# Kernel tuning notes

Hardware: AMD Instinct MI355X
Metric: run time of the kernel (lower is better)

## Reference

```python
import jax, jax.numpy as jnp
import numpy as np

# 5-tap image-gradient filter (cross-correlation taps, as in F.conv2d)
_K5 = (-1.0 / 12.0, 2.0 / 3.0, 0.0, -2.0 / 3.0, 1.0 / 12.0)
ALPHA = BETA = GAMMA = DELTA = 1.0
MASK_COST = 1.0
ENTROPY_WEIGHT = 1.0


def _pen(x):
    return jnp.sqrt(x + 1e-5)


def _filt_w(x):
    # depthwise 1x5 filter along W, padding 2 (matches F.conv2d(x, kernel_gx, padding=(0,2)))
    W = x.shape[-1]
    xp = jnp.pad(x, ((0, 0), (0, 0), (0, 0), (2, 2)))
    out = _K5[0] * xp[..., 0:W]
    for j in range(1, 5):
        out = out + _K5[j] * xp[..., j:j + W]
    return out


def _filt_h(x):
    # depthwise 5x1 filter along H, padding 2
    H = x.shape[-2]
    xp = jnp.pad(x, ((0, 0), (0, 0), (2, 2), (0, 0)))
    out = _K5[0] * xp[..., 0:H, :]
    for j in range(1, 5):
        out = out + _K5[j] * xp[..., j:j + H, :]
    return out


def _warp(img, flow):
    # Bilinear warp: sample img at (x + flow_x, y + flow_y); out-of-range taps contribute 0
    B, C, H, W = img.shape
    xq = jnp.arange(W, dtype=img.dtype)[None, None, :] + flow[:, 0]  # (B,H,W)
    yq = jnp.arange(H, dtype=img.dtype)[None, :, None] + flow[:, 1]
    x0 = jnp.floor(xq)
    y0 = jnp.floor(yq)
    wx1 = xq - x0
    wy1 = yq - y0
    img_flat = img.reshape(B, C, H * W)

    def tap(xi, yi, w):
        valid = (xi >= 0) & (xi <= W - 1) & (yi >= 0) & (yi <= H - 1)
        xc = jnp.clip(xi, 0, W - 1).astype(jnp.int32)
        yc = jnp.clip(yi, 0, H - 1).astype(jnp.int32)
        idx = (yc * W + xc).reshape(B, 1, H * W)
        vals = jnp.take_along_axis(img_flat, jnp.broadcast_to(idx, (B, C, H * W)), axis=2)
        vals = vals.reshape(B, C, H, W)
        return vals * (w * valid.astype(img.dtype))[:, None]

    return (tap(x0, y0, (1 - wx1) * (1 - wy1)) + tap(x0 + 1, y0, wx1 * (1 - wy1))
            + tap(x0, y0 + 1, (1 - wx1) * wy1) + tap(x0 + 1, y0 + 1, wx1 * wy1))


def _border_mask(flow):
    B, _, H, W = flow.shape
    Xp = jnp.arange(W, dtype=flow.dtype)[None, None, :] + flow[:, 0]
    Yp = jnp.arange(H, dtype=flow.dtype)[None, :, None] + flow[:, 1]
    mask_x = jax.nn.sigmoid(Xp + 0.5) * (1.0 - jax.nn.sigmoid(Xp - (W - 0.5)))
    mask_y = jax.nn.sigmoid(Yp + 0.5) * (1.0 - jax.nn.sigmoid(Yp - (H - 0.5)))
    return mask_x * mask_y


def _direction_terms(flow_a, flow_b, img_a, img_b):
    # energy terms for one direction (warping *_b by flow_a)
    mask = _border_mask(flow_a)
    flow_b_warp = _warp(flow_b, flow_a)
    mag = jnp.sum(flow_a ** 2 + flow_b_warp ** 2, axis=1)
    diff = flow_a + flow_b_warp
    occ = 1.0 - jax.nn.sigmoid(jnp.sum(diff ** 2, axis=1) - (0.01 * mag + 0.5))
    mask = mask * occ
    mask_term = MASK_COST * jnp.sum(1.0 - mask, axis=(1, 2)).mean()
    img_b_warp = _warp(img_b, flow_a)
    A = jnp.sum((img_a - img_b_warp) ** 2, axis=1)
    data_term = ALPHA * jnp.sum(_pen(A) * mask, axis=(1, 2)).mean()
    dx = flow_a[..., 1:] - flow_a[..., :-1]
    dy = flow_a[:, :, 1:, :] - flow_a[:, :, :-1, :]
    Bt = (jnp.pad(jnp.sum(dx ** 2, axis=1), ((0, 0), (0, 0), (0, 1)))
          + jnp.pad(jnp.sum(dy ** 2, axis=1), ((0, 0), (0, 1), (0, 0))))
    smooth_term = BETA * jnp.sum(_pen(Bt), axis=(1, 2)).mean()
    Ct = (jnp.sum((_filt_w(img_a) - _filt_w(img_b_warp)) ** 2, axis=1)
          + jnp.sum((_filt_h(img_a) - _filt_h(img_b_warp)) ** 2, axis=1))
    grad_term = GAMMA * jnp.sum(_pen(Ct) * mask, axis=(1, 2)).mean()
    D = jnp.sum(diff ** 2, axis=1)
    fb_part = DELTA * jnp.sum(_pen(D) * mask, axis=(1, 2)).mean()
    return mask_term + data_term + smooth_term + grad_term + fb_part


def _elbo_epe(meanf, log_varf, meanb, log_varb, img1, img2, target, noise_f, noise_b):
    # reparameterized flow samples (Nsamples = 1)
    flowf = meanf + jnp.exp(log_varf / 2.0) * noise_f
    flowb = meanb + jnp.exp(log_varb / 2.0) * noise_b
    energy = (_direction_terms(flowf, flowb, img1, img2)
              + _direction_terms(flowb, flowf, img2, img1))
    entropy = (jnp.sum(log_varf, axis=(1, 2, 3)) / 2
               + jnp.sum(log_varb, axis=(1, 2, 3)) / 2).mean()
    elbo = energy - ENTROPY_WEIGHT * entropy
    epe = jnp.sqrt(jnp.sum((meanf - target) ** 2, axis=1)).mean()
    return elbo, epe


def setup_inputs() -> dict:
    key = jax.random.key(0)
    ks = jax.random.split(key, 9)
    B, H, W = 8, 384, 512
    return {
        "meanf": jax.random.normal(ks[0], (B, 2, H, W), jnp.float32),
        "log_varf": jax.random.normal(ks[1], (B, 2, H, W), jnp.float32),
        "meanb": jax.random.normal(ks[2], (B, 2, H, W), jnp.float32),
        "log_varb": jax.random.normal(ks[3], (B, 2, H, W), jnp.float32),
        "img1": jax.random.uniform(ks[4], (B, 3, H, W), jnp.float32),
        "img2": jax.random.uniform(ks[5], (B, 3, H, W), jnp.float32),
        "target": jax.random.normal(ks[6], (B, 2, H, W), jnp.float32),
        "noise_f": jax.random.normal(ks[7], (B, 2, H, W), jnp.float32),
        "noise_b": jax.random.normal(ks[8], (B, 2, H, W), jnp.float32),
    }


def reference(meanf, log_varf, meanb, log_varb, img1, img2, target, noise_f, noise_b):
    elbo, epe = _elbo_epe(meanf, log_varf, meanb, log_varb, img1, img2, target, noise_f, noise_b)
    return (elbo, epe)
```

## Files before the change

kernel.cpp:

```cpp
#include <hip/hip_runtime.h>
#include <math.h>

#define BATCH 8
#define IH 384
#define IW 512
#define NPIX (IH*IW)
#define BN (BATCH*NPIX)

#define TW 64
#define TH 16
#define RW (TW+4)
#define RH (TH+4)
#define RN (RW*RH)
#define NTX (IW/TW)
#define NTY (IH/TH)
#define NB_DIR (NTX*NTY*BATCH*2)

#define HS 8
#define SH (TH+2*HS)
#define SW (TW+2*HS)
#define SF4 (SW/4)

#define NB_FLOW 1536
#define ENT_OFF NB_DIR
#define EPE_OFF (ENT_OFF + NB_FLOW)
#define PART_FLOATS 8192

__device__ __forceinline__ float frcp_(float x){ return __builtin_amdgcn_rcpf(x); }
__device__ __forceinline__ float fsqrt_(float x){ return __builtin_amdgcn_sqrtf(x); }
__device__ __forceinline__ float sigmoidf_(float x){ return frcp_(1.0f + __expf(-x)); }

__device__ __forceinline__ float block_reduce_sum(float v){
    __shared__ float s[8];
    #pragma unroll
    for (int off=32; off>0; off>>=1) v += __shfl_down(v, off);
    int lane = threadIdx.x & 63, wid = threadIdx.x >> 6;
    if (lane==0) s[wid] = v;
    __syncthreads();
    float t = 0.f;
    if (wid==0){
        int nw = (blockDim.x+63)>>6;
        t = (lane < nw) ? s[lane] : 0.f;
        #pragma unroll
        for (int off=4; off>0; off>>=1) t += __shfl_down(t, off);
    }
    __syncthreads();
    return t;
}

__global__ __launch_bounds__(256)
void flows_kernel(const float* __restrict__ meanf, const float* __restrict__ log_varf,
                  const float* __restrict__ meanb, const float* __restrict__ log_varb,
                  const float* __restrict__ target,
                  const float* __restrict__ noise_f, const float* __restrict__ noise_b,
                  float* __restrict__ flowf, float* __restrict__ flowb,
                  float* __restrict__ part)
{
    int t = blockIdx.x*blockDim.x + threadIdx.x;
    const int NP4 = NPIX/4;
    int b = t / NP4, p4 = t - b*NP4;
    size_t i0 = ((size_t)b*2*NPIX)/4 + p4;
    size_t i1 = i0 + NPIX/4;

    const float4* mf = (const float4*)meanf;  const float4* lf = (const float4*)log_varf;
    const float4* mb = (const float4*)meanb;  const float4* lb = (const float4*)log_varb;
    const float4* nf = (const float4*)noise_f; const float4* nb = (const float4*)noise_b;
    const float4* tg = (const float4*)target;
    float4* ff = (float4*)flowf; float4* fbp = (float4*)flowb;

    float4 lf0 = lf[i0], lf1 = lf[i1], lb0 = lb[i0], lb1 = lb[i1];
    float4 mf0 = mf[i0], mf1 = mf[i1], mb0 = mb[i0], mb1 = mb[i1];
    float4 nf0 = nf[i0], nf1 = nf[i1], nb0 = nb[i0], nb1 = nb[i1];

    float4 o;
    o.x = mf0.x + __expf(0.5f*lf0.x)*nf0.x; o.y = mf0.y + __expf(0.5f*lf0.y)*nf0.y;
    o.z = mf0.z + __expf(0.5f*lf0.z)*nf0.z; o.w = mf0.w + __expf(0.5f*lf0.w)*nf0.w;
    ff[i0] = o;
    o.x = mf1.x + __expf(0.5f*lf1.x)*nf1.x; o.y = mf1.y + __expf(0.5f*lf1.y)*nf1.y;
    o.z = mf1.z + __expf(0.5f*lf1.z)*nf1.z; o.w = mf1.w + __expf(0.5f*lf1.w)*nf1.w;
    ff[i1] = o;
    o.x = mb0.x + __expf(0.5f*lb0.x)*nb0.x; o.y = mb0.y + __expf(0.5f*lb0.y)*nb0.y;
    o.z = mb0.z + __expf(0.5f*lb0.z)*nb0.z; o.w = mb0.w + __expf(0.5f*lb0.w)*nb0.w;
    fbp[i0] = o;
    o.x = mb1.x + __expf(0.5f*lb1.x)*nb1.x; o.y = mb1.y + __expf(0.5f*lb1.y)*nb1.y;
    o.z = mb1.z + __expf(0.5f*lb1.z)*nb1.z; o.w = mb1.w + __expf(0.5f*lb1.w)*nb1.w;
    fbp[i1] = o;

    float ent = (lf0.x+lf0.y+lf0.z+lf0.w) + (lf1.x+lf1.y+lf1.z+lf1.w)
              + (lb0.x+lb0.y+lb0.z+lb0.w) + (lb1.x+lb1.y+lb1.z+lb1.w);

    float4 t0 = tg[i0], t1 = tg[i1];
    float d0, d1, epe = 0.f;
    d0 = mf0.x - t0.x; d1 = mf1.x - t1.x; epe += fsqrt_(d0*d0 + d1*d1);
    d0 = mf0.y - t0.y; d1 = mf1.y - t1.y; epe += fsqrt_(d0*d0 + d1*d1);
    d0 = mf0.z - t0.z; d1 = mf1.z - t1.z; epe += fsqrt_(d0*d0 + d1*d1);
    d0 = mf0.w - t0.w; d1 = mf1.w - t1.w; epe += fsqrt_(d0*d0 + d1*d1);

    float s = block_reduce_sum(ent);
    if (threadIdx.x == 0) part[ENT_OFF + blockIdx.x] = s;
    float s2 = block_reduce_sum(epe);
    if (threadIdx.x == 0) part[EPE_OFF + blockIdx.x] = s2;
}

__global__ __launch_bounds__(256)
void dir_kernel(const float* __restrict__ flowf, const float* __restrict__ flowb,
                const float* __restrict__ img1, const float* __restrict__ img2,
                float* __restrict__ part)
{
    __shared__ float sib[3][SH][SW];
    __shared__ float wlds[3][RH][RW];
    __shared__ float mlds[TH][TW];

    const int dir = blockIdx.z & 1, b = blockIdx.z >> 1;
    const float *pfa, *pfb, *pia, *pib;
    if (dir == 0){ pfa = flowf; pfb = flowb; pia = img1; pib = img2; }
    else         { pfa = flowb; pfb = flowf; pia = img2; pib = img1; }
    pfa += (size_t)b*2*NPIX; pfb += (size_t)b*2*NPIX;
    pia += (size_t)b*3*NPIX; pib += (size_t)b*3*NPIX;

    const int tw0 = blockIdx.x*TW, th0 = blockIdx.y*TH;
    const int tid = threadIdx.x;
    float local = 0.f;

    for (int i = tid; i < 3*SH*SF4; i += 256){
        int c = i / (SH*SF4);
        int rem = i - c*(SH*SF4);
        int r = rem / SF4, c4 = rem - r*SF4;
        int gy = th0 - HS + r;
        int gx = tw0 - HS + 4*c4;
        float4 v = make_float4(0.f, 0.f, 0.f, 0.f);
        if (gy >= 0 && gy < IH && gx >= 0 && gx < IW){
            v = *(const float4*)(pib + (size_t)c*NPIX + gy*IW + gx);
        }
        *(float4*)&sib[c][r][4*c4] = v;
    }
    __syncthreads();

    for (int i = tid; i < RN; i += 256){
        int hh = i / RW, ww = i - hh*RW;
        int gh = th0 + hh - 2, gw = tw0 + ww - 2;
        bool inimg = (gh >= 0) && (gh < IH) && (gw >= 0) && (gw < IW);
        float w0 = 0.f, w1 = 0.f, w2 = 0.f;
        if (inimg){
            int p = gh*IW + gw;
            float fax = pfa[p], fay = pfa[NPIX + p];
            float Xp = (float)gw + fax;
            float Yp = (float)gh + fay;

            float x0f = floorf(Xp), y0f = floorf(Yp);
            float wx1 = Xp - x0f, wy1 = Yp - y0f;
            float wx0 = 1.f - wx1, wy0 = 1.f - wy1;

            float x1f = x0f + 1.f, y1f = y0f + 1.f;
            bool vx0 = (x0f >= 0.f) && (x0f <= (float)(IW-1));
            bool vx1 = (x1f >= 0.f) && (x1f <= (float)(IW-1));
            bool vy0 = (y0f >= 0.f) && (y0f <= (float)(IH-1));
            bool vy1 = (y1f >= 0.f) && (y1f <= (float)(IH-1));
            float xc0 = fminf(fmaxf(x0f, 0.f), (float)(IW-1));
            float xc1 = fminf(fmaxf(x1f, 0.f), (float)(IW-1));
            float yc0 = fminf(fmaxf(y0f, 0.f), (float)(IH-1));
            float yc1 = fminf(fmaxf(y1f, 0.f), (float)(IH-1));
            int ix0 = (int)xc0, ix1 = (int)xc1, iy0 = (int)yc0, iy1 = (int)yc1;
            int idx0 = iy0*IW + ix0, idx1 = iy0*IW + ix1;
            int idx2 = iy1*IW + ix0, idx3 = iy1*IW + ix1;
            float wt0 = (vx0 && vy0) ? wx0*wy0 : 0.f;
            float wt1 = (vx1 && vy0) ? wx1*wy0 : 0.f;
            float wt2 = (vx0 && vy1) ? wx0*wy1 : 0.f;
            float wt3 = (vx1 && vy1) ? wx1*wy1 : 0.f;

            int lx0 = ix0 - (tw0 - HS), ly0 = iy0 - (th0 - HS);
            int lx1 = ix1 - (tw0 - HS), ly1 = iy1 - (th0 - HS);
            bool inwin = (lx0 >= 0) && (lx1 < SW) && (ly0 >= 0) && (ly1 < SH);
            if (inwin){
                int o00 = ly0*SW + lx0, o01 = ly0*SW + lx1;
                int o10 = ly1*SW + lx0, o11 = ly1*SW + lx1;
                const float* s0 = &sib[0][0][0];
                const float* s1 = s0 + SH*SW;
                const float* s2 = s1 + SH*SW;
                w0 = wt0*s0[o00] + wt1*s0[o01] + wt2*s0[o10] + wt3*s0[o11];
                w1 = wt0*s1[o00] + wt1*s1[o01] + wt2*s1[o10] + wt3*s1[o11];
                w2 = wt0*s2[o00] + wt1*s2[o01] + wt2*s2[o10] + wt3*s2[o11];
            } else {
                const float* g1 = pib + NPIX;
                const float* g2 = pib + 2*NPIX;
                w0 = wt0*pib[idx0] + wt1*pib[idx1] + wt2*pib[idx2] + wt3*pib[idx3];
                w1 = wt0*g1[idx0]  + wt1*g1[idx1]  + wt2*g1[idx2]  + wt3*g1[idx3];
                w2 = wt0*g2[idx0]  + wt1*g2[idx1]  + wt2*g2[idx2]  + wt3*g2[idx3];
            }

            bool interior = (hh >= 2) && (hh < RH-2) && (ww >= 2) && (ww < RW-2);
            if (interior){
                float mx = sigmoidf_(Xp + 0.5f) * (1.f - sigmoidf_(Xp - ((float)IW - 0.5f)));
                float my = sigmoidf_(Yp + 0.5f) * (1.f - sigmoidf_(Yp - ((float)IH - 0.5f)));
                float bm = mx * my;

                float fbwx = wt0*pfb[idx0] + wt1*pfb[idx1] + wt2*pfb[idx2] + wt3*pfb[idx3];
                const float* pfb1 = pfb + NPIX;
                float fbwy = wt0*pfb1[idx0] + wt1*pfb1[idx1] + wt2*pfb1[idx2] + wt3*pfb1[idx3];

                float mag = fax*fax + fay*fay + fbwx*fbwx + fbwy*fbwy;
                float dfx = fax + fbwx, dfy = fay + fbwy;
                float D = dfx*dfx + dfy*dfy;
                float occ = 1.f - sigmoidf_(D - (0.01f*mag + 0.5f));
                float mask = bm * occ;
                mlds[hh-2][ww-2] = mask;

                local += (1.f - mask);

                float d0 = pia[p]        - w0;
                float d1 = pia[NPIX+p]   - w1;
                float d2 = pia[2*NPIX+p] - w2;
                local += fsqrt_(d0*d0 + d1*d1 + d2*d2 + 1e-5f) * mask;

                local += fsqrt_(D + 1e-5f) * mask;

                float Bt = 0.f;
                if (gw < IW-1){
                    float e0 = pfa[p+1] - fax;
                    float e1 = pfa[NPIX + p+1] - fay;
                    Bt += e0*e0 + e1*e1;
                }
                if (gh < IH-1){
                    float e0 = pfa[p+IW] - fax;
                    float e1 = pfa[NPIX + p+IW] - fay;
                    Bt += e0*e0 + e1*e1;
                }
                local += fsqrt_(Bt + 1e-5f);
            }
        }
        wlds[0][hh][ww] = w0;
        wlds[1][hh][ww] = w1;
        wlds[2][hh][ww] = w2;
    }
    __syncthreads();

    const float K0 = -1.f/12.f, K1 = 2.f/3.f, K3 = -2.f/3.f, K4 = 1.f/12.f;
    for (int i = tid; i < TW*TH; i += 256){
        int hh = i >> 6, ww = i & 63;
        int gh = th0 + hh, gw = tw0 + ww;
        int lh = hh + 2, lw = ww + 2;
        int p = gh*IW + gw;
        float Ct = 0.f;
        #pragma unroll
        for (int c = 0; c < 3; ++c){
            const float* A_ = pia + (size_t)c*NPIX;
            float gxa = 0.f;
            if (gw >= 2)    gxa += K0*A_[p-2];
            if (gw >= 1)    gxa += K1*A_[p-1];
            if (gw <= IW-2) gxa += K3*A_[p+1];
            if (gw <= IW-3) gxa += K4*A_[p+2];
            float gxw = K0*wlds[c][lh][lw-2] + K1*wlds[c][lh][lw-1]
                      + K3*wlds[c][lh][lw+1] + K4*wlds[c][lh][lw+2];
            float d = gxa - gxw; Ct += d*d;
            float gya = 0.f;
            if (gh >= 2)    gya += K0*A_[p-2*IW];
            if (gh >= 1)    gya += K1*A_[p-IW];
            if (gh <= IH-2) gya += K3*A_[p+IW];
            if (gh <= IH-3) gya += K4*A_[p+2*IW];
            float gyw = K0*wlds[c][lh-2][lw] + K1*wlds[c][lh-1][lw]
                      + K3*wlds[c][lh+1][lw] + K4*wlds[c][lh+2][lw];
            d = gya - gyw; Ct += d*d;
        }
        local += fsqrt_(Ct + 1e-5f) * mlds[hh][ww];
    }

    float s = block_reduce_sum(local);
    if (tid == 0) part[blockIdx.x + NTX*(blockIdx.y + NTY*blockIdx.z)] = s;
}

__global__ __launch_bounds__(256)
void finalize_kernel(const float* __restrict__ part, float* __restrict__ out)
{
    float e = 0.f, ent = 0.f, epe = 0.f;
    for (int i = threadIdx.x; i < NB_DIR; i += 256) e += part[i];
    for (int i = threadIdx.x; i < NB_FLOW; i += 256){
        ent += part[ENT_OFF + i];
        epe += part[EPE_OFF + i];
    }
    e   = block_reduce_sum(e);
    ent = block_reduce_sum(ent);
    epe = block_reduce_sum(epe);
    if (threadIdx.x == 0){
        out[0] = e / (float)BATCH - ent / (2.f * (float)BATCH);
        out[1] = epe / ((float)BATCH * (float)NPIX);
    }
}

extern "C" void kernel_launch(void* const* d_in, const int* in_sizes, int n_in,
                              void* d_out, int out_size, void* d_ws, size_t ws_size,
                              hipStream_t stream)
{
    const float* meanf    = (const float*)d_in[0];
    const float* log_varf = (const float*)d_in[1];
    const float* meanb    = (const float*)d_in[2];
    const float* log_varb = (const float*)d_in[3];
    const float* img1     = (const float*)d_in[4];
    const float* img2     = (const float*)d_in[5];
    const float* target   = (const float*)d_in[6];
    const float* noise_f  = (const float*)d_in[7];
    const float* noise_b  = (const float*)d_in[8];

    float* ws    = (float*)d_ws;
    float* part  = ws;
    float* flowf = ws + PART_FLOATS;
    float* flowb = flowf + 2*(size_t)BN;

    const int threads = 256;

    flows_kernel<<<NB_FLOW, threads, 0, stream>>>(meanf, log_varf, meanb, log_varb,
                                                  target, noise_f, noise_b,
                                                  flowf, flowb, part);

    dim3 grid(NTX, NTY, BATCH*2);
    dir_kernel<<<grid, threads, 0, stream>>>(flowf, flowb, img1, img2, part);

    finalize_kernel<<<1, threads, 0, stream>>>(part, (float*)d_out);
}
```

Baseline: 274.1 us.

## Alias warp scratch onto image window LDS and prefetch flow into registers

After: 267.2 us. 2.5% less time.

```diff
diff --git a/kernel.cpp b/kernel.cpp
--- a/kernel.cpp
+++ b/kernel.cpp
@@ -16,10 +16,13 @@
 #define NTY (IH/TH)
 #define NB_DIR (NTX*NTY*BATCH*2)
 
-#define HS 8
-#define SH (TH+2*HS)
-#define SW (TW+2*HS)
+#define HSX 8
+#define HSY 6
+#define SH (TH+2*HSY)
+#define SW (TW+2*HSX)
 #define SF4 (SW/4)
+#define SMEM_FLOATS (3*SH*SW)
+#define NITER 6
 
 #define NB_FLOW 1536
 #define ENT_OFF NB_DIR
@@ -102,13 +105,12 @@
     if (threadIdx.x == 0) part[EPE_OFF + blockIdx.x] = s2;
 }
 
-__global__ __launch_bounds__(256)
+__global__ __launch_bounds__(256, 5)
 void dir_kernel(const float* __restrict__ flowf, const float* __restrict__ flowb,
                 const float* __restrict__ img1, const float* __restrict__ img2,
                 float* __restrict__ part)
 {
-    __shared__ float sib[3][SH][SW];
-    __shared__ float wlds[3][RH][RW];
+    __shared__ float smem[SMEM_FLOATS];
     __shared__ float mlds[TH][TW];
 
     const int dir = blockIdx.z & 1, b = blockIdx.z >> 1;
@@ -126,115 +128,149 @@
         int c = i / (SH*SF4);
         int rem = i - c*(SH*SF4);
         int r = rem / SF4, c4 = rem - r*SF4;
-        int gy = th0 - HS + r;
-        int gx = tw0 - HS + 4*c4;
+        int gy = th0 - HSY + r;
+        int gx = tw0 - HSX + 4*c4;
         float4 v = make_float4(0.f, 0.f, 0.f, 0.f);
         if (gy >= 0 && gy < IH && gx >= 0 && gx < IW){
             v = *(const float4*)(pib + (size_t)c*NPIX + gy*IW + gx);
         }
-        *(float4*)&sib[c][r][4*c4] = v;
-    }
-    __syncthreads();
-
-    for (int i = tid; i < RN; i += 256){
+        *(float4*)&smem[c*(SH*SW) + r*SW + 4*c4] = v;
+    }
+
+    float rfax[NITER], rfay[NITER];
+    #pragma unroll
+    for (int it = 0; it < NITER; ++it){
+        rfax[it] = 0.f; rfay[it] = 0.f;
+        int i = tid + it*256;
+        if (i < RN){
+            int hh = i / RW, ww = i - hh*RW;
+            int gh = th0 + hh - 2, gw = tw0 + ww - 2;
+            if (gh >= 0 && gh < IH && gw >= 0 && gw < IW){
+                int p = gh*IW + gw;
+                rfax[it] = pfa[p];
+                rfay[it] = pfa[NPIX + p];
+            }
+        }
+    }
+    __syncthreads();
+
+    float rw0[NITER], rw1[NITER], rw2[NITER];
+    #pragma unroll
+    for (int it = 0; it < NITER; ++it){
+        rw0[it] = 0.f; rw1[it] = 0.f; rw2[it] = 0.f;
+        int i = tid + it*256;
+        if (i >= RN) continue;
         int hh = i / RW, ww = i - hh*RW;
         int gh = th0 + hh - 2, gw = tw0 + ww - 2;
         bool inimg = (gh >= 0) && (gh < IH) && (gw >= 0) && (gw < IW);
-        float w0 = 0.f, w1 = 0.f, w2 = 0.f;
-        if (inimg){
-            int p = gh*IW + gw;
-            float fax = pfa[p], fay = pfa[NPIX + p];
-            float Xp = (float)gw + fax;
-            float Yp = (float)gh + fay;
-
-            float x0f = floorf(Xp), y0f = floorf(Yp);
-            float wx1 = Xp - x0f, wy1 = Yp - y0f;
-            float wx0 = 1.f - wx1, wy0 = 1.f - wy1;
-
-            float x1f = x0f + 1.f, y1f = y0f + 1.f;
-            bool vx0 = (x0f >= 0.f) && (x0f <= (float)(IW-1));
-            bool vx1 = (x1f >= 0.f) && (x1f <= (float)(IW-1));
-            bool vy0 = (y0f >= 0.f) && (y0f <= (float)(IH-1));
-            bool vy1 = (y1f >= 0.f) && (y1f <= (float)(IH-1));
-            float xc0 = fminf(fmaxf(x0f, 0.f), (float)(IW-1));
-            float xc1 = fminf(fmaxf(x1f, 0.f), (float)(IW-1));
-            float yc0 = fminf(fmaxf(y0f, 0.f), (float)(IH-1));
-            float yc1 = fminf(fmaxf(y1f, 0.f), (float)(IH-1));
-            int ix0 = (int)xc0, ix1 = (int)xc1, iy0 = (int)yc0, iy1 = (int)yc1;
-            int idx0 = iy0*IW + ix0, idx1 = iy0*IW + ix1;
-            int idx2 = iy1*IW + ix0, idx3 = iy1*IW + ix1;
-            float wt0 = (vx0 && vy0) ? wx0*wy0 : 0.f;
-            float wt1 = (vx1 && vy0) ? wx1*wy0 : 0.f;
-            float wt2 = (vx0 && vy1) ? wx0*wy1 : 0.f;
-            float wt3 = (vx1 && vy1) ? wx1*wy1 : 0.f;
-
-            int lx0 = ix0 - (tw0 - HS), ly0 = iy0 - (th0 - HS);
-            int lx1 = ix1 - (tw0 - HS), ly1 = iy1 - (th0 - HS);
-            bool inwin = (lx0 >= 0) && (lx1 < SW) && (ly0 >= 0) && (ly1 < SH);
-            if (inwin){
-                int o00 = ly0*SW + lx0, o01 = ly0*SW + lx1;
-                int o10 = ly1*SW + lx0, o11 = ly1*SW + lx1;
-                const float* s0 = &sib[0][0][0];
-                const float* s1 = s0 + SH*SW;
-                const float* s2 = s1 + SH*SW;
-                w0 = wt0*s0[o00] + wt1*s0[o01] + wt2*s0[o10] + wt3*s0[o11];
-                w1 = wt0*s1[o00] + wt1*s1[o01] + wt2*s1[o10] + wt3*s1[o11];
-                w2 = wt0*s2[o00] + wt1*s2[o01] + wt2*s2[o10] + wt3*s2[o11];
-            } else {
-                const float* g1 = pib + NPIX;
-                const float* g2 = pib + 2*NPIX;
-                w0 = wt0*pib[idx0] + wt1*pib[idx1] + wt2*pib[idx2] + wt3*pib[idx3];
-                w1 = wt0*g1[idx0]  + wt1*g1[idx1]  + wt2*g1[idx2]  + wt3*g1[idx3];
-                w2 = wt0*g2[idx0]  + wt1*g2[idx1]  + wt2*g2[idx2]  + wt3*g2[idx3];
+        if (!inimg) continue;
+
+        int p = gh*IW + gw;
+        float fax = rfax[it], fay = rfay[it];
+        float Xp = (float)gw + fax;
+        float Yp = (float)gh + fay;
+
+        float x0f = floorf(Xp), y0f = floorf(Yp);
+        float wx1 = Xp - x0f, wy1 = Yp - y0f;
+        float wx0 = 1.f - wx1, wy0 = 1.f - wy1;
+
+        float x1f = x0f + 1.f, y1f = y0f + 1.f;
+        bool vx0 = (x0f >= 0.f) && (x0f <= (float)(IW-1));
+        bool vx1 = (x1f >= 0.f) && (x1f <= (float)(IW-1));
+        bool vy0 = (y0f >= 0.f) && (y0f <= (float)(IH-1));
+        bool vy1 = (y1f >= 0.f) && (y1f <= (float)(IH-1));
+        float xc0 = fminf(fmaxf(x0f, 0.f), (float)(IW-1));
+        float xc1 = fminf(fmaxf(x1f, 0.f), (float)(IW-1));
+        float yc0 = fminf(fmaxf(y0f, 0.f), (float)(IH-1));
+        float yc1 = fminf(fmaxf(y1f, 0.f), (float)(IH-1));
+        int ix0 = (int)xc0, ix1 = (int)xc1, iy0 = (int)yc0, iy1 = (int)yc1;
+        int idx0 = iy0*IW + ix0, idx1 = iy0*IW + ix1;
+        int idx2 = iy1*IW + ix0, idx3 = iy1*IW + ix1;
+        float wt0 = (vx0 && vy0) ? wx0*wy0 : 0.f;
+        float wt1 = (vx1 && vy0) ? wx1*wy0 : 0.f;
+        float wt2 = (vx0 && vy1) ? wx0*wy1 : 0.f;
+        float wt3 = (vx1 && vy1) ? wx1*wy1 : 0.f;
+
+        float w0, w1, w2;
+        int lx0 = ix0 - (tw0 - HSX), ly0 = iy0 - (th0 - HSY);
+        int lx1 = ix1 - (tw0 - HSX), ly1 = iy1 - (th0 - HSY);
+        bool inwin = (lx0 >= 0) && (lx1 < SW) && (ly0 >= 0) && (ly1 < SH);
+        if (inwin){
+            int o00 = ly0*SW + lx0, o01 = ly0*SW + lx1;
+            int o10 = ly1*SW + lx0, o11 = ly1*SW + lx1;
+            const float* s0 = &smem[0];
+            const float* s1 = s0 + SH*SW;
+            const float* s2 = s1 + SH*SW;
+            w0 = wt0*s0[o00] + wt1*s0[o01] + wt2*s0[o10] + wt3*s0[o11];
+            w1 = wt0*s1[o00] + wt1*s1[o01] + wt2*s1[o10] + wt3*s1[o11];
+            w2 = wt0*s2[o00] + wt1*s2[o01] + wt2*s2[o10] + wt3*s2[o11];
+        } else {
+            const float* g1 = pib + NPIX;
+            const float* g2 = pib + 2*NPIX;
+            w0 = wt0*pib[idx0] + wt1*pib[idx1] + wt2*pib[idx2] + wt3*pib[idx3];
+            w1 = wt0*g1[idx0]  + wt1*g1[idx1]  + wt2*g1[idx2]  + wt3*g1[idx3];
+            w2 = wt0*g2[idx0]  + wt1*g2[idx1]  + wt2*g2[idx2]  + wt3*g2[idx3];
+        }
+        rw0[it] = w0; rw1[it] = w1; rw2[it] = w2;
+
+        bool interior = (hh >= 2) && (hh < RH-2) && (ww >= 2) && (ww < RW-2);
+        if (interior){
+            float mx = sigmoidf_(Xp + 0.5f) * (1.f - sigmoidf_(Xp - ((float)IW - 0.5f)));
+            float my = sigmoidf_(Yp + 0.5f) * (1.f - sigmoidf_(Yp - ((float)IH - 0.5f)));
+            float bm = mx * my;
+
+            float fbwx = wt0*pfb[idx0] + wt1*pfb[idx1] + wt2*pfb[idx2] + wt3*pfb[idx3];
+            const float* pfb1 = pfb + NPIX;
+            float fbwy = wt0*pfb1[idx0] + wt1*pfb1[idx1] + wt2*pfb1[idx2] + wt3*pfb1[idx3];
+
+            float mag = fax*fax + fay*fay + fbwx*fbwx + fbwy*fbwy;
+            float dfx = fax + fbwx, dfy = fay + fbwy;
+            float D = dfx*dfx + dfy*dfy;
+            float occ = 1.f - sigmoidf_(D - (0.01f*mag + 0.5f));
+            float mask = bm * occ;
+            mlds[hh-2][ww-2] = mask;
+
+            local += (1.f - mask);
+
+            float d0 = pia[p]        - w0;
+            float d1 = pia[NPIX+p]   - w1;
+            float d2 = pia[2*NPIX+p] - w2;
+            local += fsqrt_(d0*d0 + d1*d1 + d2*d2 + 1e-5f) * mask;
+
+            local += fsqrt_(D + 1e-5f) * mask;
+
+            float Bt = 0.f;
+            if (gw < IW-1){
+                float e0 = pfa[p+1] - fax;
+                float e1 = pfa[NPIX + p+1] - fay;
+                Bt += e0*e0 + e1*e1;
             }
-
-            bool interior = (hh >= 2) && (hh < RH-2) && (ww >= 2) && (ww < RW-2);
-            if (interior){
-                float mx = sigmoidf_(Xp + 0.5f) * (1.f - sigmoidf_(Xp - ((float)IW - 0.5f)));
-                float my = sigmoidf_(Yp + 0.5f) * (1.f - sigmoidf_(Yp - ((float)IH - 0.5f)));
-                float bm = mx * my;
-
-                float fbwx = wt0*pfb[idx0] + wt1*pfb[idx1] + wt2*pfb[idx2] + wt3*pfb[idx3];
-                const float* pfb1 = pfb + NPIX;
-                float fbwy = wt0*pfb1[idx0] + wt1*pfb1[idx1] + wt2*pfb1[idx2] + wt3*pfb1[idx3];
-
-                float mag = fax*fax + fay*fay + fbwx*fbwx + fbwy*fbwy;
-                float dfx = fax + fbwx, dfy = fay + fbwy;
-                float D = dfx*dfx + dfy*dfy;
-                float occ = 1.f - sigmoidf_(D - (0.01f*mag + 0.5f));
-                float mask = bm * occ;
-                mlds[hh-2][ww-2] = mask;
-
-                local += (1.f - mask);
-
-                float d0 = pia[p]        - w0;
-                float d1 = pia[NPIX+p]   - w1;
-                float d2 = pia[2*NPIX+p] - w2;
-                local += fsqrt_(d0*d0 + d1*d1 + d2*d2 + 1e-5f) * mask;
-
-                local += fsqrt_(D + 1e-5f) * mask;
-
-                float Bt = 0.f;
-                if (gw < IW-1){
-                    float e0 = pfa[p+1] - fax;
-                    float e1 = pfa[NPIX + p+1] - fay;
-                    Bt += e0*e0 + e1*e1;
-                }
-                if (gh < IH-1){
-                    float e0 = pfa[p+IW] - fax;
-                    float e1 = pfa[NPIX + p+IW] - fay;
-                    Bt += e0*e0 + e1*e1;
-                }
-                local += fsqrt_(Bt + 1e-5f);
+            if (gh < IH-1){
+                float e0 = pfa[p+IW] - fax;
+                float e1 = pfa[NPIX + p+IW] - fay;
+                Bt += e0*e0 + e1*e1;
             }
-        }
-        wlds[0][hh][ww] = w0;
-        wlds[1][hh][ww] = w1;
-        wlds[2][hh][ww] = w2;
+            local += fsqrt_(Bt + 1e-5f);
+        }
+    }
+    __syncthreads();
+
+    #pragma unroll
+    for (int it = 0; it < NITER; ++it){
+        int i = tid + it*256;
+        if (i < RN){
+            int hh = i / RW, ww = i - hh*RW;
+            smem[0*(RH*RW) + hh*RW + ww] = rw0[it];
+            smem[1*(RH*RW) + hh*RW + ww] = rw1[it];
+            smem[2*(RH*RW) + hh*RW + ww] = rw2[it];
+        }
     }
     __syncthreads();
 
     const float K0 = -1.f/12.f, K1 = 2.f/3.f, K3 = -2.f/3.f, K4 = 1.f/12.f;
+    const float* wl0 = &smem[0];
+    const float* wl1 = wl0 + RH*RW;
+    const float* wl2 = wl1 + RH*RW;
     for (int i = tid; i < TW*TH; i += 256){
         int hh = i >> 6, ww = i & 63;
         int gh = th0 + hh, gw = tw0 + ww;
@@ -244,21 +280,22 @@
         #pragma unroll
         for (int c = 0; c < 3; ++c){
             const float* A_ = pia + (size_t)c*NPIX;
+            const float* Wl = (c == 0) ? wl0 : (c == 1) ? wl1 : wl2;
             float gxa = 0.f;
             if (gw >= 2)    gxa += K0*A_[p-2];
             if (gw >= 1)    gxa += K1*A_[p-1];
             if (gw <= IW-2) gxa += K3*A_[p+1];
             if (gw <= IW-3) gxa += K4*A_[p+2];
-            float gxw = K0*wlds[c][lh][lw-2] + K1*wlds[c][lh][lw-1]
-                      + K3*wlds[c][lh][lw+1] + K4*wlds[c][lh][lw+2];
+            float gxw = K0*Wl[lh*RW + lw-2] + K1*Wl[lh*RW + lw-1]
+                      + K3*Wl[lh*RW + lw+1] + K4*Wl[lh*RW + lw+2];
             float d = gxa - gxw; Ct += d*d;
             float gya = 0.f;
             if (gh >= 2)    gya += K0*A_[p-2*IW];
             if (gh >= 1)    gya += K1*A_[p-IW];
             if (gh <= IH-2) gya += K3*A_[p+IW];
             if (gh <= IH-3) gya += K4*A_[p+2*IW];
-            float gyw = K0*wlds[c][lh-2][lw] + K1*wlds[c][lh-1][lw]
-                      + K3*wlds[c][lh+1][lw] + K4*wlds[c][lh+2][lw];
+            float gyw = K0*Wl[(lh-2)*RW + lw] + K1*Wl[(lh-1)*RW + lw]
+                      + K3*Wl[(lh+1)*RW + lw] + K4*Wl[(lh+2)*RW + lw];
             d = gya - gyw; Ct += d*d;
         }
         local += fsqrt_(Ct + 1e-5f) * mlds[hh][ww];
```

## Split direction kernel into warp and gradient passes with interleaved flow layout

Applied to the files above, without the earlier changes.

After: 247.7 us. 1.11x faster.

```diff
diff --git a/kernel.cpp b/kernel.cpp
--- a/kernel.cpp
+++ b/kernel.cpp
@@ -11,20 +11,25 @@
 #define TH 16
 #define RW (TW+4)
 #define RH (TH+4)
-#define RN (RW*RH)
 #define NTX (IW/TW)
 #define NTY (IH/TH)
-#define NB_DIR (NTX*NTY*BATCH*2)
-
-#define HS 8
-#define SH (TH+2*HS)
-#define SW (TW+2*HS)
+#define NZ  (BATCH*2)
+#define NB_DIR (NTX*NTY*NZ)
+
+#define HSX 8
+#define HSY 6
+#define SH (TH+2*HSY)
+#define SW (TW+2*HSX)
 #define SF4 (SW/4)
 
+#define NITER_A 4
+
 #define NB_FLOW 1536
-#define ENT_OFF NB_DIR
+#define PA_OFF 0
+#define PB_OFF NB_DIR
+#define ENT_OFF (2*NB_DIR)
 #define EPE_OFF (ENT_OFF + NB_FLOW)
-#define PART_FLOATS 8192
+#define PART_FLOATS 16384
 
 __device__ __forceinline__ float frcp_(float x){ return __builtin_amdgcn_rcpf(x); }
 __device__ __forceinline__ float fsqrt_(float x){ return __builtin_amdgcn_sqrtf(x); }
@@ -57,6 +62,7 @@
                   float* __restrict__ part)
 {
     int t = blockIdx.x*blockDim.x + threadIdx.x;
+    if (t < NB_DIR) part[PB_OFF + t] = 0.f;
     const int NP4 = NPIX/4;
     int b = t / NP4, p4 = t - b*NP4;
     size_t i0 = ((size_t)b*2*NPIX)/4 + p4;
@@ -72,19 +78,23 @@
     float4 mf0 = mf[i0], mf1 = mf[i1], mb0 = mb[i0], mb1 = mb[i1];
     float4 nf0 = nf[i0], nf1 = nf[i1], nb0 = nb[i0], nb1 = nb[i1];
 
-    float4 o;
-    o.x = mf0.x + __expf(0.5f*lf0.x)*nf0.x; o.y = mf0.y + __expf(0.5f*lf0.y)*nf0.y;
-    o.z = mf0.z + __expf(0.5f*lf0.z)*nf0.z; o.w = mf0.w + __expf(0.5f*lf0.w)*nf0.w;
-    ff[i0] = o;
-    o.x = mf1.x + __expf(0.5f*lf1.x)*nf1.x; o.y = mf1.y + __expf(0.5f*lf1.y)*nf1.y;
-    o.z = mf1.z + __expf(0.5f*lf1.z)*nf1.z; o.w = mf1.w + __expf(0.5f*lf1.w)*nf1.w;
-    ff[i1] = o;
-    o.x = mb0.x + __expf(0.5f*lb0.x)*nb0.x; o.y = mb0.y + __expf(0.5f*lb0.y)*nb0.y;
-    o.z = mb0.z + __expf(0.5f*lb0.z)*nb0.z; o.w = mb0.w + __expf(0.5f*lb0.w)*nb0.w;
-    fbp[i0] = o;
-    o.x = mb1.x + __expf(0.5f*lb1.x)*nb1.x; o.y = mb1.y + __expf(0.5f*lb1.y)*nb1.y;
-    o.z = mb1.z + __expf(0.5f*lb1.z)*nb1.z; o.w = mb1.w + __expf(0.5f*lb1.w)*nb1.w;
-    fbp[i1] = o;
+    float4 of0, of1;
+    of0.x = mf0.x + __expf(0.5f*lf0.x)*nf0.x; of0.y = mf0.y + __expf(0.5f*lf0.y)*nf0.y;
+    of0.z = mf0.z + __expf(0.5f*lf0.z)*nf0.z; of0.w = mf0.w + __expf(0.5f*lf0.w)*nf0.w;
+    of1.x = mf1.x + __expf(0.5f*lf1.x)*nf1.x; of1.y = mf1.y + __expf(0.5f*lf1.y)*nf1.y;
+    of1.z = mf1.z + __expf(0.5f*lf1.z)*nf1.z; of1.w = mf1.w + __expf(0.5f*lf1.w)*nf1.w;
+    float4 ob0, ob1;
+    ob0.x = mb0.x + __expf(0.5f*lb0.x)*nb0.x; ob0.y = mb0.y + __expf(0.5f*lb0.y)*nb0.y;
+    ob0.z = mb0.z + __expf(0.5f*lb0.z)*nb0.z; ob0.w = mb0.w + __expf(0.5f*lb0.w)*nb0.w;
+    ob1.x = mb1.x + __expf(0.5f*lb1.x)*nb1.x; ob1.y = mb1.y + __expf(0.5f*lb1.y)*nb1.y;
+    ob1.z = mb1.z + __expf(0.5f*lb1.z)*nb1.z; ob1.w = mb1.w + __expf(0.5f*lb1.w)*nb1.w;
+
+    size_t o4 = (size_t)b*(NPIX/2) + (size_t)p4*2;
+    float4 v;
+    v.x = of0.x; v.y = of1.x; v.z = of0.y; v.w = of1.y; ff[o4]   = v;
+    v.x = of0.z; v.y = of1.z; v.z = of0.w; v.w = of1.w; ff[o4+1] = v;
+    v.x = ob0.x; v.y = ob1.x; v.z = ob0.y; v.w = ob1.y; fbp[o4]   = v;
+    v.x = ob0.z; v.y = ob1.z; v.z = ob0.w; v.w = ob1.w; fbp[o4+1] = v;
 
     float ent = (lf0.x+lf0.y+lf0.z+lf0.w) + (lf1.x+lf1.y+lf1.z+lf1.w)
               + (lb0.x+lb0.y+lb0.z+lb0.w) + (lb1.x+lb1.y+lb1.z+lb1.w);
@@ -102,21 +112,30 @@
     if (threadIdx.x == 0) part[EPE_OFF + blockIdx.x] = s2;
 }
 
-__global__ __launch_bounds__(256)
-void dir_kernel(const float* __restrict__ flowf, const float* __restrict__ flowb,
-                const float* __restrict__ img1, const float* __restrict__ img2,
-                float* __restrict__ part)
+__global__ __launch_bounds__(256, 6)
+void dirA_kernel(const float* __restrict__ flowf, const float* __restrict__ flowb,
+                 const float* __restrict__ img1, const float* __restrict__ img2,
+                 float* __restrict__ wimg, float* __restrict__ maskbuf,
+                 float* __restrict__ part)
 {
     __shared__ float sib[3][SH][SW];
-    __shared__ float wlds[3][RH][RW];
-    __shared__ float mlds[TH][TW];
-
-    const int dir = blockIdx.z & 1, b = blockIdx.z >> 1;
-    const float *pfa, *pfb, *pia, *pib;
-    if (dir == 0){ pfa = flowf; pfb = flowb; pia = img1; pib = img2; }
-    else         { pfa = flowb; pfb = flowf; pia = img2; pib = img1; }
-    pfa += (size_t)b*2*NPIX; pfb += (size_t)b*2*NPIX;
-    pia += (size_t)b*3*NPIX; pib += (size_t)b*3*NPIX;
+
+    const int z = blockIdx.z;
+    const int dir = z & 1, b = z >> 1;
+    const float2 *pfa2, *pfb2;
+    const float *pia, *pib;
+    if (dir == 0){
+        pfa2 = (const float2*)flowf + (size_t)b*NPIX;
+        pfb2 = (const float2*)flowb + (size_t)b*NPIX;
+        pia = img1 + (size_t)b*3*NPIX; pib = img2 + (size_t)b*3*NPIX;
+    } else {
+        pfa2 = (const float2*)flowb + (size_t)b*NPIX;
+        pfb2 = (const float2*)flowf + (size_t)b*NPIX;
+        pia = img2 + (size_t)b*3*NPIX; pib = img1 + (size_t)b*3*NPIX;
+    }
+
+    float* wout = wimg + (size_t)z*3*NPIX;
+    float* mout = maskbuf + (size_t)z*NPIX;
 
     const int tw0 = blockIdx.x*TW, th0 = blockIdx.y*TH;
     const int tid = threadIdx.x;
@@ -126,153 +145,198 @@
         int c = i / (SH*SF4);
         int rem = i - c*(SH*SF4);
         int r = rem / SF4, c4 = rem - r*SF4;
-        int gy = th0 - HS + r;
-        int gx = tw0 - HS + 4*c4;
+        int gy = th0 - HSY + r;
+        int gx = tw0 - HSX + 4*c4;
         float4 v = make_float4(0.f, 0.f, 0.f, 0.f);
         if (gy >= 0 && gy < IH && gx >= 0 && gx < IW){
             v = *(const float4*)(pib + (size_t)c*NPIX + gy*IW + gx);
         }
         *(float4*)&sib[c][r][4*c4] = v;
     }
+
+    float2 rfa[NITER_A];
+    #pragma unroll
+    for (int it = 0; it < NITER_A; ++it){
+        int i = tid + it*256;
+        int hh = i >> 6, ww = i & 63;
+        int p = (th0 + hh)*IW + (tw0 + ww);
+        rfa[it] = pfa2[p];
+    }
     __syncthreads();
 
-    for (int i = tid; i < RN; i += 256){
-        int hh = i / RW, ww = i - hh*RW;
-        int gh = th0 + hh - 2, gw = tw0 + ww - 2;
-        bool inimg = (gh >= 0) && (gh < IH) && (gw >= 0) && (gw < IW);
-        float w0 = 0.f, w1 = 0.f, w2 = 0.f;
-        if (inimg){
-            int p = gh*IW + gw;
-            float fax = pfa[p], fay = pfa[NPIX + p];
-            float Xp = (float)gw + fax;
-            float Yp = (float)gh + fay;
-
-            float x0f = floorf(Xp), y0f = floorf(Yp);
-            float wx1 = Xp - x0f, wy1 = Yp - y0f;
-            float wx0 = 1.f - wx1, wy0 = 1.f - wy1;
-
-            float x1f = x0f + 1.f, y1f = y0f + 1.f;
-            bool vx0 = (x0f >= 0.f) && (x0f <= (float)(IW-1));
-            bool vx1 = (x1f >= 0.f) && (x1f <= (float)(IW-1));
-            bool vy0 = (y0f >= 0.f) && (y0f <= (float)(IH-1));
-            bool vy1 = (y1f >= 0.f) && (y1f <= (float)(IH-1));
-            float xc0 = fminf(fmaxf(x0f, 0.f), (float)(IW-1));
-            float xc1 = fminf(fmaxf(x1f, 0.f), (float)(IW-1));
-            float yc0 = fminf(fmaxf(y0f, 0.f), (float)(IH-1));
-            float yc1 = fminf(fmaxf(y1f, 0.f), (float)(IH-1));
-            int ix0 = (int)xc0, ix1 = (int)xc1, iy0 = (int)yc0, iy1 = (int)yc1;
-            int idx0 = iy0*IW + ix0, idx1 = iy0*IW + ix1;
-            int idx2 = iy1*IW + ix0, idx3 = iy1*IW + ix1;
-            float wt0 = (vx0 && vy0) ? wx0*wy0 : 0.f;
-            float wt1 = (vx1 && vy0) ? wx1*wy0 : 0.f;
-            float wt2 = (vx0 && vy1) ? wx0*wy1 : 0.f;
-            float wt3 = (vx1 && vy1) ? wx1*wy1 : 0.f;
-
-            int lx0 = ix0 - (tw0 - HS), ly0 = iy0 - (th0 - HS);
-            int lx1 = ix1 - (tw0 - HS), ly1 = iy1 - (th0 - HS);
-            bool inwin = (lx0 >= 0) && (lx1 < SW) && (ly0 >= 0) && (ly1 < SH);
-            if (inwin){
-                int o00 = ly0*SW + lx0, o01 = ly0*SW + lx1;
-                int o10 = ly1*SW + lx0, o11 = ly1*SW + lx1;
-                const float* s0 = &sib[0][0][0];
-                const float* s1 = s0 + SH*SW;
-                const float* s2 = s1 + SH*SW;
-                w0 = wt0*s0[o00] + wt1*s0[o01] + wt2*s0[o10] + wt3*s0[o11];
-                w1 = wt0*s1[o00] + wt1*s1[o01] + wt2*s1[o10] + wt3*s1[o11];
-                w2 = wt0*s2[o00] + wt1*s2[o01] + wt2*s2[o10] + wt3*s2[o11];
-            } else {
-                const float* g1 = pib + NPIX;
-                const float* g2 = pib + 2*NPIX;
-                w0 = wt0*pib[idx0] + wt1*pib[idx1] + wt2*pib[idx2] + wt3*pib[idx3];
-                w1 = wt0*g1[idx0]  + wt1*g1[idx1]  + wt2*g1[idx2]  + wt3*g1[idx3];
-                w2 = wt0*g2[idx0]  + wt1*g2[idx1]  + wt2*g2[idx2]  + wt3*g2[idx3];
-            }
-
-            bool interior = (hh >= 2) && (hh < RH-2) && (ww >= 2) && (ww < RW-2);
-            if (interior){
-                float mx = sigmoidf_(Xp + 0.5f) * (1.f - sigmoidf_(Xp - ((float)IW - 0.5f)));
-                float my = sigmoidf_(Yp + 0.5f) * (1.f - sigmoidf_(Yp - ((float)IH - 0.5f)));
-                float bm = mx * my;
-
-                float fbwx = wt0*pfb[idx0] + wt1*pfb[idx1] + wt2*pfb[idx2] + wt3*pfb[idx3];
-                const float* pfb1 = pfb + NPIX;
-                float fbwy = wt0*pfb1[idx0] + wt1*pfb1[idx1] + wt2*pfb1[idx2] + wt3*pfb1[idx3];
-
-                float mag = fax*fax + fay*fay + fbwx*fbwx + fbwy*fbwy;
-                float dfx = fax + fbwx, dfy = fay + fbwy;
-                float D = dfx*dfx + dfy*dfy;
-                float occ = 1.f - sigmoidf_(D - (0.01f*mag + 0.5f));
-                float mask = bm * occ;
-                mlds[hh-2][ww-2] = mask;
-
-                local += (1.f - mask);
-
-                float d0 = pia[p]        - w0;
-                float d1 = pia[NPIX+p]   - w1;
-                float d2 = pia[2*NPIX+p] - w2;
-                local += fsqrt_(d0*d0 + d1*d1 + d2*d2 + 1e-5f) * mask;
-
-                local += fsqrt_(D + 1e-5f) * mask;
-
-                float Bt = 0.f;
-                if (gw < IW-1){
-                    float e0 = pfa[p+1] - fax;
-                    float e1 = pfa[NPIX + p+1] - fay;
-                    Bt += e0*e0 + e1*e1;
-                }
-                if (gh < IH-1){
-                    float e0 = pfa[p+IW] - fax;
-                    float e1 = pfa[NPIX + p+IW] - fay;
-                    Bt += e0*e0 + e1*e1;
-                }
-                local += fsqrt_(Bt + 1e-5f);
-            }
-        }
-        wlds[0][hh][ww] = w0;
-        wlds[1][hh][ww] = w1;
-        wlds[2][hh][ww] = w2;
-    }
-    __syncthreads();
-
-    const float K0 = -1.f/12.f, K1 = 2.f/3.f, K3 = -2.f/3.f, K4 = 1.f/12.f;
-    for (int i = tid; i < TW*TH; i += 256){
+    #pragma unroll
+    for (int it = 0; it < NITER_A; ++it){
+        int i = tid + it*256;
         int hh = i >> 6, ww = i & 63;
         int gh = th0 + hh, gw = tw0 + ww;
+        int p = gh*IW + gw;
+        float fax = rfa[it].x, fay = rfa[it].y;
+        float Xp = (float)gw + fax;
+        float Yp = (float)gh + fay;
+
+        float2 f_r = (gw < IW-1) ? pfa2[p+1]  : make_float2(0.f, 0.f);
+        float2 f_d = (gh < IH-1) ? pfa2[p+IW] : make_float2(0.f, 0.f);
+
+        float x0f = floorf(Xp), y0f = floorf(Yp);
+        float wx1 = Xp - x0f, wy1 = Yp - y0f;
+        float wx0 = 1.f - wx1, wy0 = 1.f - wy1;
+
+        float x1f = x0f + 1.f, y1f = y0f + 1.f;
+        bool vx0 = (x0f >= 0.f) && (x0f <= (float)(IW-1));
+        bool vx1 = (x1f >= 0.f) && (x1f <= (float)(IW-1));
+        bool vy0 = (y0f >= 0.f) && (y0f <= (float)(IH-1));
+        bool vy1 = (y1f >= 0.f) && (y1f <= (float)(IH-1));
+        float xc0 = fminf(fmaxf(x0f, 0.f), (float)(IW-1));
+        float xc1 = fminf(fmaxf(x1f, 0.f), (float)(IW-1));
+        float yc0 = fminf(fmaxf(y0f, 0.f), (float)(IH-1));
+        float yc1 = fminf(fmaxf(y1f, 0.f), (float)(IH-1));
+        int ix0 = (int)xc0, ix1 = (int)xc1, iy0 = (int)yc0, iy1 = (int)yc1;
+        int idx0 = iy0*IW + ix0, idx1 = iy0*IW + ix1;
+        int idx2 = iy1*IW + ix0, idx3 = iy1*IW + ix1;
+        float wt0 = (vx0 && vy0) ? wx0*wy0 : 0.f;
+        float wt1 = (vx1 && vy0) ? wx1*wy0 : 0.f;
+        float wt2 = (vx0 && vy1) ? wx0*wy1 : 0.f;
+        float wt3 = (vx1 && vy1) ? wx1*wy1 : 0.f;
+
+        float2 fb0 = pfb2[idx0], fb1 = pfb2[idx1];
+        float2 fb2 = pfb2[idx2], fb3 = pfb2[idx3];
+
+        float a0 = pia[p], a1 = pia[NPIX+p], a2 = pia[2*NPIX+p];
+
+        float w0, w1, w2;
+        int lx0 = ix0 - (tw0 - HSX), ly0 = iy0 - (th0 - HSY);
+        int lx1 = ix1 - (tw0 - HSX), ly1 = iy1 - (th0 - HSY);
+        bool inwin = (lx0 >= 0) && (lx1 < SW) && (ly0 >= 0) && (ly1 < SH);
+        if (inwin){
+            int o00 = ly0*SW + lx0, o01 = ly0*SW + lx1;
+            int o10 = ly1*SW + lx0, o11 = ly1*SW + lx1;
+            const float* s0 = &sib[0][0][0];
+            const float* s1 = s0 + SH*SW;
+            const float* s2 = s1 + SH*SW;
+            w0 = wt0*s0[o00] + wt1*s0[o01] + wt2*s0[o10] + wt3*s0[o11];
+            w1 = wt0*s1[o00] + wt1*s1[o01] + wt2*s1[o10] + wt3*s1[o11];
+            w2 = wt0*s2[o00] + wt1*s2[o01] + wt2*s2[o10] + wt3*s2[o11];
+        } else {
+            const float* g1 = pib + NPIX;
+            const float* g2 = pib + 2*NPIX;
+            w0 = wt0*pib[idx0] + wt1*pib[idx1] + wt2*pib[idx2] + wt3*pib[idx3];
+            w1 = wt0*g1[idx0]  + wt1*g1[idx1]  + wt2*g1[idx2]  + wt3*g1[idx3];
+            w2 = wt0*g2[idx0]  + wt1*g2[idx1]  + wt2*g2[idx2]  + wt3*g2[idx3];
+        }
+
+        float mx = sigmoidf_(Xp + 0.5f) * (1.f - sigmoidf_(Xp - ((float)IW - 0.5f)));
+        float my = sigmoidf_(Yp + 0.5f) * (1.f - sigmoidf_(Yp - ((float)IH - 0.5f)));
+        float bm = mx * my;
+
+        float fbwx = wt0*fb0.x + wt1*fb1.x + wt2*fb2.x + wt3*fb3.x;
+        float fbwy = wt0*fb0.y + wt1*fb1.y + wt2*fb2.y + wt3*fb3.y;
+
+        float mag = fax*fax + fay*fay + fbwx*fbwx + fbwy*fbwy;
+        float dfx = fax + fbwx, dfy = fay + fbwy;
+        float D = dfx*dfx + dfy*dfy;
+        float occ = 1.f - sigmoidf_(D - (0.01f*mag + 0.5f));
+        float mask = bm * occ;
+
+        local += (1.f - mask);
+
+        float d0 = a0 - w0;
+        float d1 = a1 - w1;
+        float d2 = a2 - w2;
+        local += fsqrt_(d0*d0 + d1*d1 + d2*d2 + 1e-5f) * mask;
+
+        local += fsqrt_(D + 1e-5f) * mask;
+
+        float Bt = 0.f;
+        if (gw < IW-1){
+            float e0 = f_r.x - fax;
+            float e1 = f_r.y - fay;
+            Bt += e0*e0 + e1*e1;
+        }
+        if (gh < IH-1){
+            float e0 = f_d.x - fax;
+            float e1 = f_d.y - fay;
+            Bt += e0*e0 + e1*e1;
+        }
+        local += fsqrt_(Bt + 1e-5f);
+
+        wout[p]          = w0;
+        wout[NPIX + p]   = w1;
+        wout[2*NPIX + p] = w2;
+        mout[p]          = mask;
+    }
+
+    float s = block_reduce_sum(local);
+    if (tid == 0) part[PA_OFF + blockIdx.x + NTX*(blockIdx.y + NTY*blockIdx.z)] = s;
+}
+
+__global__ __launch_bounds__(256, 4)
+void dirB_kernel(const float* __restrict__ img1, const float* __restrict__ img2,
+                 const float* __restrict__ wimg, const float* __restrict__ maskbuf,
+                 float* __restrict__ part)
+{
+    __shared__ float wt[3][RH][RW];
+    __shared__ float at[3][RH][RW];
+
+    const int z = blockIdx.z;
+    const int dir = z & 1, b = z >> 1;
+    const float* pia = ((dir == 0) ? img1 : img2) + (size_t)b*3*NPIX;
+    const float* wsrc = wimg + (size_t)z*3*NPIX;
+    const float* msrc = maskbuf + (size_t)z*NPIX;
+
+    const int tw0 = blockIdx.x*TW, th0 = blockIdx.y*TH;
+    const int tid = threadIdx.x;
+    float local = 0.f;
+
+    for (int i = tid; i < 3*RH*RW; i += 256){
+        int c = i / (RH*RW);
+        int rem = i - c*(RH*RW);
+        int r = rem / RW, cc = rem - r*RW;
+        int gy = th0 + r - 2;
+        int gx = tw0 + cc - 2;
+        float va = 0.f, vw = 0.f;
+        if (gy >= 0 && gy < IH && gx >= 0 && gx < IW){
+            size_t q = (size_t)c*NPIX + gy*IW + gx;
+            va = pia[q];
+            vw = wsrc[q];
+        }
+        at[c][r][cc] = va;
+        wt[c][r][cc] = vw;
+    }
+    __syncthreads();
+
+    const float K0 = -1.f/12.f, K1 = 2.f/3.f, K3 = -2.f/3.f, K4 = 1.f/12.f;
+    #pragma unroll
+    for (int it = 0; it < NITER_A; ++it){
+        int i = tid + it*256;
+        int hh = i >> 6, ww = i & 63;
+        int p = (th0 + hh)*IW + (tw0 + ww);
         int lh = hh + 2, lw = ww + 2;
-        int p = gh*IW + gw;
         float Ct = 0.f;
         #pragma unroll
         for (int c = 0; c < 3; ++c){
-            const float* A_ = pia + (size_t)c*NPIX;
-            float gxa = 0.f;
-            if (gw >= 2)    gxa += K0*A_[p-2];
-            if (gw >= 1)    gxa += K1*A_[p-1];
-            if (gw <= IW-2) gxa += K3*A_[p+1];
-            if (gw <= IW-3) gxa += K4*A_[p+2];
-            float gxw = K0*wlds[c][lh][lw-2] + K1*wlds[c][lh][lw-1]
-                      + K3*wlds[c][lh][lw+1] + K4*wlds[c][lh][lw+2];
+            float gxa = K0*at[c][lh][lw-2] + K1*at[c][lh][lw-1]
+                      + K3*at[c][lh][lw+1] + K4*at[c][lh][lw+2];
+            float gxw = K0*wt[c][lh][lw-2] + K1*wt[c][lh][lw-1]
+                      + K3*wt[c][lh][lw+1] + K4*wt[c][lh][lw+2];
             float d = gxa - gxw; Ct += d*d;
-            float gya = 0.f;
-            if (gh >= 2)    gya += K0*A_[p-2*IW];
-            if (gh >= 1)    gya += K1*A_[p-IW];
-            if (gh <= IH-2) gya += K3*A_[p+IW];
-            if (gh <= IH-3) gya += K4*A_[p+2*IW];
-            float gyw = K0*wlds[c][lh-2][lw] + K1*wlds[c][lh-1][lw]
-                      + K3*wlds[c][lh+1][lw] + K4*wlds[c][lh+2][lw];
+            float gya = K0*at[c][lh-2][lw] + K1*at[c][lh-1][lw]
+                      + K3*at[c][lh+1][lw] + K4*at[c][lh+2][lw];
+            float gyw = K0*wt[c][lh-2][lw] + K1*wt[c][lh-1][lw]
+                      + K3*wt[c][lh+1][lw] + K4*wt[c][lh+2][lw];
             d = gya - gyw; Ct += d*d;
         }
-        local += fsqrt_(Ct + 1e-5f) * mlds[hh][ww];
+        local += fsqrt_(Ct + 1e-5f) * msrc[p];
     }
 
     float s = block_reduce_sum(local);
-    if (tid == 0) part[blockIdx.x + NTX*(blockIdx.y + NTY*blockIdx.z)] = s;
+    if (tid == 0) part[PB_OFF + blockIdx.x + NTX*(blockIdx.y + NTY*blockIdx.z)] = s;
 }
 
 __global__ __launch_bounds__(256)
 void finalize_kernel(const float* __restrict__ part, float* __restrict__ out)
 {
     float e = 0.f, ent = 0.f, epe = 0.f;
-    for (int i = threadIdx.x; i < NB_DIR; i += 256) e += part[i];
+    for (int i = threadIdx.x; i < 2*NB_DIR; i += 256) e += part[i];
     for (int i = threadIdx.x; i < NB_FLOW; i += 256){
         ent += part[ENT_OFF + i];
         epe += part[EPE_OFF + i];
@@ -304,6 +368,8 @@
     float* part  = ws;
     float* flowf = ws + PART_FLOATS;
     float* flowb = flowf + 2*(size_t)BN;
+    float* wimg  = flowb + 2*(size_t)BN;
+    float* maskb = wimg + (size_t)NZ*3*NPIX;
 
     const int threads = 256;
 
@@ -311,8 +377,10 @@
                                                   target, noise_f, noise_b,
                                                   flowf, flowb, part);
 
-    dim3 grid(NTX, NTY, BATCH*2);
-    dir_kernel<<<grid, threads, 0, stream>>>(flowf, flowb, img1, img2, part);
+    dim3 grid(NTX, NTY, NZ);
+    dirA_kernel<<<grid, threads, 0, stream>>>(flowf, flowb, img1, img2,
+                                              wimg, maskb, part);
+    dirB_kernel<<<grid, threads, 0, stream>>>(img1, img2, wimg, maskb, part);
 
     finalize_kernel<<<1, threads, 0, stream>>>(part, (float*)d_out);
 }
```
